# Optimization experiments

Measured on AMD Instinct MI355X. Metric: run time of the kernel, lower is better.

## Reference

```python
import jax, jax.numpy as jnp
import numpy as np

EMB, HEADS = 1024, 16
S = EMB // HEADS  # per-head dim = 64


def setup_inputs() -> dict:
    key = jax.random.key(0)
    ks = jax.random.split(key, 7)
    b, t = 2, 2048
    sc = 0.02
    return {
        "x": jax.random.normal(ks[0], (b, t, EMB), jnp.float32),
        "W_down": jax.random.normal(ks[1], (EMB, EMB), jnp.float32) * sc,
        "tokeys": jax.random.normal(ks[2], (HEADS, S, S), jnp.float32) * sc,
        "toqueries": jax.random.normal(ks[3], (HEADS, S, S), jnp.float32) * sc,
        "tovalues": jax.random.normal(ks[4], (HEADS, S, S), jnp.float32) * sc,
        "W_unify": jax.random.normal(ks[5], (EMB, EMB), jnp.float32) * sc,
        "b_unify": jax.random.normal(ks[6], (EMB,), jnp.float32) * sc,
    }


def reference(x, W_down, tokeys, toqueries, tovalues, W_unify, b_unify):
    b, t, e = x.shape
    h, s = HEADS, S
    scale = s ** (-0.25)
    # downproj (bias-free linear), split into heads: [b,t,h,s]
    xd = (x @ W_down).reshape(b, t, h, s)
    # per-head s x s projections
    keys = jnp.einsum("bthk,hik->bthi", xd, tokeys) * scale
    queries = jnp.einsum("bthk,hik->bthi", xd, toqueries) * scale
    values = jnp.einsum("bthk,hik->bthi", xd, tovalues)
    # attention: scores [b,h,q,k]
    dot = jnp.einsum("bqhs,bkhs->bhqk", queries, keys)
    attn = jax.nn.softmax(dot, axis=-1)
    out = jnp.einsum("bhqk,bkhs->bqhs", attn, values).reshape(b, t, e)
    return out @ W_unify + b_unify
```

## Files before the change

### kernel.cpp

```cpp
#include <hip/hip_runtime.h>

#define EMB   1024
#define HEADS 16
#define SDIM  64
#define BATCH 2
#define TSEQ  2048
#define BT    (BATCH*TSEQ)
#define NBH   (BATCH*HEADS)

typedef __attribute__((ext_vector_type(8))) short short8;
typedef __attribute__((ext_vector_type(4))) float f32x4;

static __device__ __forceinline__ unsigned short f2bf(float f) {
  unsigned u = __builtin_bit_cast(unsigned, f);
  u = (u + 0x7FFFu + ((u >> 16) & 1u)) >> 16;
  return (unsigned short)u;
}

#define MFMA(a, b, c) __builtin_amdgcn_mfma_f32_16x16x32_bf16((a), (b), (c), 0, 0, 0)

#define GLOAD_LDS16(g, l)                                                     \
  __builtin_amdgcn_global_load_lds(                                           \
      (const __attribute__((address_space(1))) unsigned*)(g),                 \
      (__attribute__((address_space(3))) unsigned*)(l), 16, 0, 0)

__global__ __launch_bounds__(256) void convert_kernel(
    const float* __restrict__ x,
    const float* __restrict__ tk, const float* __restrict__ tq,
    const float* __restrict__ tv,
    unsigned short* __restrict__ xb,
    unsigned short* __restrict__ pk, unsigned short* __restrict__ pq,
    unsigned short* __restrict__ pv) {
  const int NX4 = BT * EMB / 4;
  const int NP4 = HEADS * SDIM * SDIM / 4;
  int i = blockIdx.x * blockDim.x + threadIdx.x;
  const float* src; unsigned short* dst; int off;
  if (i < NX4)               { src = x;  dst = xb; off = i * 4; }
  else if (i < NX4 + NP4)    { src = tk; dst = pk; off = (i - NX4) * 4; }
  else if (i < NX4 + 2*NP4)  { src = tq; dst = pq; off = (i - NX4 - NP4) * 4; }
  else if (i < NX4 + 3*NP4)  { src = tv; dst = pv; off = (i - NX4 - 2*NP4) * 4; }
  else return;
  float4 v = *(const float4*)(src + off);
  ushort4 o;
  o.x = f2bf(v.x); o.y = f2bf(v.y); o.z = f2bf(v.z); o.w = f2bf(v.w);
  *(ushort4*)(dst + off) = o;
}

__global__ __launch_bounds__(256) void transpose_w_kernel(
    const float* __restrict__ w0, const float* __restrict__ w1,
    unsigned short* __restrict__ o0, unsigned short* __restrict__ o1) {
  __shared__ float tile[32][33];
  const float* in        = blockIdx.z ? w1 : w0;
  unsigned short* out    = blockIdx.z ? o1 : o0;
  int r0 = blockIdx.y * 32, c0 = blockIdx.x * 32;
  int tid = threadIdx.x;
  int r = tid >> 3, c4 = (tid & 7) * 4;
  float4 v = *(const float4*)(in + (size_t)(r0 + r) * EMB + c0 + c4);
  tile[r][c4 + 0] = v.x; tile[r][c4 + 1] = v.y;
  tile[r][c4 + 2] = v.z; tile[r][c4 + 3] = v.w;
  __syncthreads();
  ushort4 o;
  o.x = f2bf(tile[c4 + 0][r]);
  o.y = f2bf(tile[c4 + 1][r]);
  o.z = f2bf(tile[c4 + 2][r]);
  o.w = f2bf(tile[c4 + 3][r]);
  *(ushort4*)(out + (size_t)(c0 + r) * EMB + r0 + c4) = o;
}

template <int MODE>
__global__ __launch_bounds__(256) void gemm_bt_kernel(
    const unsigned short* __restrict__ A,
    const unsigned short* __restrict__ Bt,
    unsigned short* __restrict__ Cbf, float* __restrict__ Cf,
    const float* __restrict__ bias) {
  __shared__ short As[64 * 32];
  __shared__ short Bs[128 * 32];
  const int tid = threadIdx.x;
  const int lane = tid & 63;
  const int w = __builtin_amdgcn_readfirstlane(tid >> 6);
  const int wr = w >> 1, wc = w & 1;
  const int l15 = lane & 15, l4 = lane >> 4;
  const int flat = blockIdx.y * gridDim.x + blockIdx.x;
  const int vid = (flat & 7) * 64 + (flat >> 3);
  const int m0 = (vid >> 3) * 64;
  const int n0 = (vid & 7) * 128;
  const int lrow = lane >> 2, lcol = (lane & 3) * 8;
  f32x4 acc[2][4] = {};
  for (int kt = 0; kt < 32; ++kt) {
    const int k0 = kt * 32;
    for (int i = 0; i < 3; ++i) {
      int c = w * 3 + i;
      if (c < 4) {
        GLOAD_LDS16(A + (size_t)(m0 + c * 16 + lrow) * EMB + k0 + lcol,
                    &As[c * 512]);
      } else {
        int cb = c - 4;
        GLOAD_LDS16(Bt + (size_t)(n0 + cb * 16 + lrow) * EMB + k0 + lcol,
                    &Bs[cb * 512]);
      }
    }
    __syncthreads();
    short8 af[2], bf[4];
    for (int mi = 0; mi < 2; ++mi)
      af[mi] = *(short8*)&As[(wr * 32 + mi * 16 + l15) * 32 + l4 * 8];
    for (int ni = 0; ni < 4; ++ni)
      bf[ni] = *(short8*)&Bs[(wc * 64 + ni * 16 + l15) * 32 + l4 * 8];
    __builtin_amdgcn_s_setprio(1);
    for (int mi = 0; mi < 2; ++mi)
      for (int ni = 0; ni < 4; ++ni)
        acc[mi][ni] = MFMA(af[mi], bf[ni], acc[mi][ni]);
    __builtin_amdgcn_s_setprio(0);
    __syncthreads();
  }
  for (int mi = 0; mi < 2; ++mi)
    for (int ni = 0; ni < 4; ++ni) {
      int col = n0 + wc * 64 + ni * 16 + l15;
      for (int r = 0; r < 4; ++r) {
        int row = m0 + wr * 32 + mi * 16 + l4 * 4 + r;
        if (MODE == 0)
          Cbf[(size_t)row * EMB + col] = f2bf(acc[mi][ni][r]);
        else
          Cf[(size_t)row * EMB + col] = acc[mi][ni][r] + bias[col];
      }
    }
}

__global__ __launch_bounds__(256) void proj_qkv_kernel(
    const unsigned short* __restrict__ XD,
    const unsigned short* __restrict__ PK, const unsigned short* __restrict__ PQ,
    const unsigned short* __restrict__ PV,
    unsigned short* __restrict__ Qg, unsigned short* __restrict__ Kg,
    unsigned short* __restrict__ Vt) {
  __shared__ short xs[64 * 72];
  __shared__ short ps[3][64 * 72];
  const int tid = threadIdx.x, lane = tid & 63;
  const int w = __builtin_amdgcn_readfirstlane(tid >> 6);
  const int tt = blockIdx.x, bh = blockIdx.y;
  const int b = bh >> 4, h = bh & 15;
  const int l15 = lane & 15, l4 = lane >> 4;
  const unsigned short* srcs[3] = {PK + h * 4096, PQ + h * 4096, PV + h * 4096};
  for (int u = tid; u < 512; u += 256) {
    int row = u >> 3, ch = (u & 7) * 8;
    *(short8*)&xs[row * 72 + ch] = *(const short8*)(
        XD + (size_t)(b * TSEQ + tt * 64 + row) * EMB + h * 64 + ch);
  }
  for (int m = 0; m < 3; ++m)
    for (int u = tid; u < 512; u += 256) {
      int row = u >> 3, ch = (u & 7) * 8;
      *(short8*)&ps[m][row * 72 + ch] = *(const short8*)(srcs[m] + row * 64 + ch);
    }
  __syncthreads();
  short8 af[2];
  af[0] = *(short8*)&xs[(w * 16 + l15) * 72 + l4 * 8];
  af[1] = *(short8*)&xs[(w * 16 + l15) * 72 + 32 + l4 * 8];
  f32x4 aK[4] = {}, aQ[4] = {}, aV[4] = {};
  for (int ni = 0; ni < 4; ++ni)
    for (int kc = 0; kc < 2; ++kc) {
      short8 bk = *(short8*)&ps[0][(ni * 16 + l15) * 72 + kc * 32 + l4 * 8];
      short8 bq = *(short8*)&ps[1][(ni * 16 + l15) * 72 + kc * 32 + l4 * 8];
      short8 bv = *(short8*)&ps[2][(ni * 16 + l15) * 72 + kc * 32 + l4 * 8];
      aK[ni] = MFMA(af[kc], bk, aK[ni]);
      aQ[ni] = MFMA(af[kc], bq, aQ[ni]);
      aV[ni] = MFMA(af[kc], bv, aV[ni]);
    }
  for (int ni = 0; ni < 4; ++ni)
    for (int r = 0; r < 4; ++r) {
      int t = tt * 64 + w * 16 + l4 * 4 + r;
      size_t o = (size_t)(bh * TSEQ + t) * SDIM + ni * 16 + l15;
      Qg[o] = f2bf(aQ[ni][r]);
      Kg[o] = f2bf(aK[ni][r]);
    }
  __syncthreads();
  for (int ni = 0; ni < 4; ++ni)
    for (int r = 0; r < 4; ++r)
      xs[(w * 16 + l4 * 4 + r) * 72 + ni * 16 + l15] = (short)f2bf(aV[ni][r]);
  __syncthreads();
  for (int u = tid; u < 512; u += 256) {
    int d = u >> 3, ch = (u & 7) * 8;
    short8 v;
    for (int e = 0; e < 8; ++e) v[e] = xs[(ch + e) * 72 + d];
    *(short8*)(Vt + (size_t)(bh * 64 + d) * TSEQ + tt * 64 + ch) = v;
  }
}

__global__ __launch_bounds__(256) void attn_kernel(
    const unsigned short* __restrict__ Qg, const unsigned short* __restrict__ Kg,
    const unsigned short* __restrict__ Vt, unsigned short* __restrict__ Og) {
  __shared__ short Ks[2][64 * 64];
  __shared__ short Vs[2][64 * 64];
  __shared__ short Ps[4][16 * 64];
  const int tid = threadIdx.x, lane = tid & 63;
  const int w = __builtin_amdgcn_readfirstlane(tid >> 6);
  const int flat = blockIdx.y * gridDim.x + blockIdx.x;
  const int vid = (flat & 7) * 128 + (flat >> 3);
  const int qt = vid & 31, bh = vid >> 5;
  const int b = bh >> 4, h = bh & 15;
  const int l15 = lane & 15, l4 = lane >> 4;
  short8 qf[2];
  {
    int row = qt * 64 + w * 16 + l15;
    const unsigned short* qp = Qg + (size_t)(bh * TSEQ + row) * SDIM;
    qf[0] = *(const short8*)(qp + l4 * 8);
    qf[1] = *(const short8*)(qp + 32 + l4 * 8);
  }
  const unsigned short* Kbase = Kg + (size_t)bh * TSEQ * SDIM;
  const unsigned short* Vbase = Vt + (size_t)bh * SDIM * TSEQ;
  const int ur = tid >> 3, uc = (tid & 7);
  float lsum[4] = {0.f, 0.f, 0.f, 0.f};
  f32x4 O[4] = {};
  short8 rk0, rk1, rv0, rv1;
  auto loadKV = [&](int kt) {
    rk0 = *(const short8*)(Kbase + (size_t)(kt * 64 + ur) * SDIM + uc * 8);
    rk1 = *(const short8*)(Kbase + (size_t)(kt * 64 + ur + 32) * SDIM + uc * 8);
    rv0 = *(const short8*)(Vbase + (size_t)ur * TSEQ + kt * 64 + uc * 8);
    rv1 = *(const short8*)(Vbase + (size_t)(ur + 32) * TSEQ + kt * 64 + uc * 8);
  };
  auto storeKV = [&](int c) {
    char* KB = (char*)Ks[c]; char* VB = (char*)Vs[c];
    const int chB = uc * 16;
    *(short8*)(KB + ((ur * 128 + chB) ^ ((ur & 7) << 4)))        = rk0;
    *(short8*)(KB + (((ur + 32) * 128 + chB) ^ ((ur & 7) << 4))) = rk1;
    *(short8*)(VB + ((ur * 128 + chB) ^ ((ur & 7) << 4)))        = rv0;
    *(short8*)(VB + (((ur + 32) * 128 + chB) ^ ((ur & 7) << 4))) = rv1;
  };
  loadKV(0);
  storeKV(0);
  int cur = 0;
  char* PB = (char*)Ps[w];
  for (int kt = 0; kt < 32; ++kt) {
    __syncthreads();
    if (kt < 31) loadKV(kt + 1);
    char* KB = (char*)Ks[cur]; char* VB = (char*)Vs[cur];
    f32x4 s[4] = {};
    __builtin_amdgcn_s_setprio(1);
    for (int ni = 0; ni < 4; ++ni) {
      int j = ni * 16 + l15, sw = (j & 7) << 4;
      short8 kf0 = *(short8*)(KB + ((j * 128 + l4 * 16) ^ sw));
      short8 kf1 = *(short8*)(KB + ((j * 128 + 64 + l4 * 16) ^ sw));
      s[ni] = MFMA(qf[0], kf0, s[ni]);
      s[ni] = MFMA(qf[1], kf1, s[ni]);
    }
    __builtin_amdgcn_s_setprio(0);
    for (int ni = 0; ni < 4; ++ni)
      for (int r = 0; r < 4; ++r) {
        float p = __expf(s[ni][r] * 0.125f);
        lsum[r] += p;
        int row = l4 * 4 + r;
        *(unsigned short*)(PB + ((row * 128 + (ni * 16 + l15) * 2) ^
                                 ((row & 7) << 4))) = f2bf(p);
      }
    short8 pf0, pf1;
    {
      int sw = (l15 & 7) << 4;
      pf0 = *(short8*)(PB + ((l15 * 128 + l4 * 16) ^ sw));
      pf1 = *(short8*)(PB + ((l15 * 128 + 64 + l4 * 16) ^ sw));
    }
    __builtin_amdgcn_s_setprio(1);
    for (int ni = 0; ni < 4; ++ni) {
      int dd = ni * 16 + l15, sw = (dd & 7) << 4;
      short8 vf0 = *(short8*)(VB + ((dd * 128 + l4 * 16) ^ sw));
      short8 vf1 = *(short8*)(VB + ((dd * 128 + 64 + l4 * 16) ^ sw));
      O[ni] = MFMA(pf0, vf0, O[ni]);
      O[ni] = MFMA(pf1, vf1, O[ni]);
    }
    __builtin_amdgcn_s_setprio(0);
    if (kt < 31) storeKV(cur ^ 1);
    cur ^= 1;
  }
  for (int r = 0; r < 4; ++r) {
    float t = lsum[r];
    t += __shfl_xor(t, 1); t += __shfl_xor(t, 2);
    t += __shfl_xor(t, 4); t += __shfl_xor(t, 8);
    float inv = 1.0f / t;
    int trow = qt * 64 + w * 16 + l4 * 4 + r;
    for (int ni = 0; ni < 4; ++ni)
      Og[(size_t)(b * TSEQ + trow) * EMB + h * 64 + ni * 16 + l15] =
          f2bf(O[ni][r] * inv);
  }
}

extern "C" void kernel_launch(void* const* d_in, const int* in_sizes, int n_in,
                              void* d_out, int out_size, void* d_ws, size_t ws_size,
                              hipStream_t stream) {
  const float* x  = (const float*)d_in[0];
  const float* Wd = (const float*)d_in[1];
  const float* tk = (const float*)d_in[2];
  const float* tq = (const float*)d_in[3];
  const float* tv = (const float*)d_in[4];
  const float* Wu = (const float*)d_in[5];
  const float* bu = (const float*)d_in[6];
  float* out = (float*)d_out;

  char* ws = (char*)d_ws;
  size_t off = 0;
  auto alloc = [&](size_t bytes) {
    void* p = ws + off;
    off += (bytes + 255) & ~(size_t)255;
    return p;
  };
  unsigned short* XB  = (unsigned short*)alloc((size_t)BT * EMB * 2);
  unsigned short* WDT = (unsigned short*)alloc((size_t)EMB * EMB * 2);
  unsigned short* WUT = (unsigned short*)alloc((size_t)EMB * EMB * 2);
  unsigned short* PKb = (unsigned short*)alloc((size_t)HEADS * SDIM * SDIM * 2);
  unsigned short* PQb = (unsigned short*)alloc((size_t)HEADS * SDIM * SDIM * 2);
  unsigned short* PVb = (unsigned short*)alloc((size_t)HEADS * SDIM * SDIM * 2);
  unsigned short* XD  = (unsigned short*)alloc((size_t)BT * EMB * 2);
  unsigned short* Qg  = (unsigned short*)alloc((size_t)NBH * TSEQ * SDIM * 2);
  unsigned short* Kg  = (unsigned short*)alloc((size_t)NBH * TSEQ * SDIM * 2);
  unsigned short* Vtr = (unsigned short*)alloc((size_t)NBH * SDIM * TSEQ * 2);
  unsigned short* Og  = (unsigned short*)alloc((size_t)BT * EMB * 2);

  const int NX4 = BT * EMB / 4, NP4 = HEADS * SDIM * SDIM / 4;
  int nconv = (NX4 + 3 * NP4 + 255) / 256;
  convert_kernel<<<nconv, 256, 0, stream>>>(x, tk, tq, tv, XB, PKb, PQb, PVb);
  transpose_w_kernel<<<dim3(32, 32, 2), 256, 0, stream>>>(Wd, Wu, WDT, WUT);
  gemm_bt_kernel<0><<<dim3(8, 64), 256, 0, stream>>>(XB, WDT, XD, nullptr, nullptr);
  proj_qkv_kernel<<<dim3(32, 32), 256, 0, stream>>>(XD, PKb, PQb, PVb, Qg, Kg, Vtr);
  attn_kernel<<<dim3(32, 32), 256, 0, stream>>>(Qg, Kg, Vtr, Og);
  gemm_bt_kernel<1><<<dim3(8, 64), 256, 0, stream>>>(Og, WUT, nullptr, out, bu);
}
```

Measured before the change: 205.0 us.

## Stream K/V fragments from global into registers and double query rows per warp

The attention kernel no longer stages K and V tiles through shared memory. Each wave now loads its MFMA K/V fragments straight from global memory into registers, prefetching the next tile, and computes 32 query rows instead of 16, so the grid is halved. Keys are permuted so that four probabilities can be packed into a single 8-byte LDS store, and exp is folded into exp2 with a combined constant. The V-transpose write in the projection kernel is also reworked to use vector LDS reads. The trade-off is that every wave fetches the same K/V data from global memory (relying on cache hits), register pressure rises under launch_bounds(256,2), and bf16 rounding becomes round-half-up.

Result: slower. 250.6 us (+22.3%).

```diff
diff --git a/kernel.cpp b/kernel.cpp
--- a/kernel.cpp
+++ b/kernel.cpp
@@ -10,11 +10,15 @@
 
 typedef __attribute__((ext_vector_type(8))) short short8;
 typedef __attribute__((ext_vector_type(4))) float f32x4;
+typedef __attribute__((ext_vector_type(2))) unsigned u32x2;
 
 static __device__ __forceinline__ unsigned short f2bf(float f) {
   unsigned u = __builtin_bit_cast(unsigned, f);
   u = (u + 0x7FFFu + ((u >> 16) & 1u)) >> 16;
   return (unsigned short)u;
+}
+static __device__ __forceinline__ unsigned bfrnd(float a) {
+  return __builtin_bit_cast(unsigned, a) + 0x8000u;
 }
 
 #define MFMA(a, b, c) __builtin_amdgcn_mfma_f32_16x16x32_bf16((a), (b), (c), 0, 0, 0)
@@ -173,110 +177,102 @@
   __syncthreads();
   for (int ni = 0; ni < 4; ++ni)
     for (int r = 0; r < 4; ++r)
-      xs[(w * 16 + l4 * 4 + r) * 72 + ni * 16 + l15] = (short)f2bf(aV[ni][r]);
+      xs[(ni * 16 + l15) * 72 + (w * 16 + l4 * 4 + r)] = (short)f2bf(aV[ni][r]);
   __syncthreads();
   for (int u = tid; u < 512; u += 256) {
     int d = u >> 3, ch = (u & 7) * 8;
-    short8 v;
-    for (int e = 0; e < 8; ++e) v[e] = xs[(ch + e) * 72 + d];
+    short8 v = *(short8*)&xs[d * 72 + ch];
     *(short8*)(Vt + (size_t)(bh * 64 + d) * TSEQ + tt * 64 + ch) = v;
   }
 }
 
-__global__ __launch_bounds__(256) void attn_kernel(
+__global__ __launch_bounds__(256, 2) void attn_kernel(
     const unsigned short* __restrict__ Qg, const unsigned short* __restrict__ Kg,
     const unsigned short* __restrict__ Vt, unsigned short* __restrict__ Og) {
-  __shared__ short Ks[2][64 * 64];
-  __shared__ short Vs[2][64 * 64];
-  __shared__ short Ps[4][16 * 64];
+  __shared__ short Ps[4][32 * 64];
   const int tid = threadIdx.x, lane = tid & 63;
   const int w = __builtin_amdgcn_readfirstlane(tid >> 6);
-  const int flat = blockIdx.y * gridDim.x + blockIdx.x;
-  const int vid = (flat & 7) * 128 + (flat >> 3);
-  const int qt = vid & 31, bh = vid >> 5;
+  const int flat = blockIdx.y * 16 + blockIdx.x;
+  const int vid = (flat & 7) * 64 + (flat >> 3);
+  const int qt = vid & 15, bh = vid >> 4;
   const int b = bh >> 4, h = bh & 15;
   const int l15 = lane & 15, l4 = lane >> 4;
-  short8 qf[2];
-  {
-    int row = qt * 64 + w * 16 + l15;
-    const unsigned short* qp = Qg + (size_t)(bh * TSEQ + row) * SDIM;
-    qf[0] = *(const short8*)(qp + l4 * 8);
-    qf[1] = *(const short8*)(qp + 32 + l4 * 8);
-  }
-  const unsigned short* Kbase = Kg + (size_t)bh * TSEQ * SDIM;
-  const unsigned short* Vbase = Vt + (size_t)bh * SDIM * TSEQ;
-  const int ur = tid >> 3, uc = (tid & 7);
-  float lsum[4] = {0.f, 0.f, 0.f, 0.f};
-  f32x4 O[4] = {};
-  short8 rk0, rk1, rv0, rv1;
-  auto loadKV = [&](int kt) {
-    rk0 = *(const short8*)(Kbase + (size_t)(kt * 64 + ur) * SDIM + uc * 8);
-    rk1 = *(const short8*)(Kbase + (size_t)(kt * 64 + ur + 32) * SDIM + uc * 8);
-    rv0 = *(const short8*)(Vbase + (size_t)ur * TSEQ + kt * 64 + uc * 8);
-    rv1 = *(const short8*)(Vbase + (size_t)(ur + 32) * TSEQ + kt * 64 + uc * 8);
-  };
-  auto storeKV = [&](int c) {
-    char* KB = (char*)Ks[c]; char* VB = (char*)Vs[c];
-    const int chB = uc * 16;
-    *(short8*)(KB + ((ur * 128 + chB) ^ ((ur & 7) << 4)))        = rk0;
-    *(short8*)(KB + (((ur + 32) * 128 + chB) ^ ((ur & 7) << 4))) = rk1;
-    *(short8*)(VB + ((ur * 128 + chB) ^ ((ur & 7) << 4)))        = rv0;
-    *(short8*)(VB + (((ur + 32) * 128 + chB) ^ ((ur & 7) << 4))) = rv1;
-  };
-  loadKV(0);
-  storeKV(0);
-  int cur = 0;
+  const int qbase = qt * 128 + w * 32;
+  short8 qf[2][2];
+  for (int h2 = 0; h2 < 2; ++h2) {
+    const unsigned short* qp =
+        Qg + (size_t)(bh * TSEQ + qbase + h2 * 16 + l15) * SDIM;
+    qf[h2][0] = *(const short8*)(qp + l4 * 8);
+    qf[h2][1] = *(const short8*)(qp + 32 + l4 * 8);
+  }
+  const unsigned short* Kp =
+      Kg + (size_t)bh * TSEQ * SDIM + (size_t)(4 * l15) * SDIM + l4 * 8;
+  const unsigned short* Vp =
+      Vt + (size_t)bh * SDIM * TSEQ + (size_t)l15 * TSEQ + l4 * 8;
+  short8 kf[4][2], vf[4][2];
+  for (int ni = 0; ni < 4; ++ni)
+    for (int kc = 0; kc < 2; ++kc) {
+      kf[ni][kc] = *(const short8*)(Kp + ni * SDIM + kc * 32);
+      vf[ni][kc] = *(const short8*)(Vp + (size_t)ni * 16 * TSEQ + kc * 32);
+    }
+  float lsum[2][4] = {};
+  f32x4 O[2][4] = {};
   char* PB = (char*)Ps[w];
+  const float CEXP = 0.18033688011112042f;
   for (int kt = 0; kt < 32; ++kt) {
-    __syncthreads();
-    if (kt < 31) loadKV(kt + 1);
-    char* KB = (char*)Ks[cur]; char* VB = (char*)Vs[cur];
-    f32x4 s[4] = {};
-    __builtin_amdgcn_s_setprio(1);
-    for (int ni = 0; ni < 4; ++ni) {
-      int j = ni * 16 + l15, sw = (j & 7) << 4;
-      short8 kf0 = *(short8*)(KB + ((j * 128 + l4 * 16) ^ sw));
-      short8 kf1 = *(short8*)(KB + ((j * 128 + 64 + l4 * 16) ^ sw));
-      s[ni] = MFMA(qf[0], kf0, s[ni]);
-      s[ni] = MFMA(qf[1], kf1, s[ni]);
-    }
-    __builtin_amdgcn_s_setprio(0);
-    for (int ni = 0; ni < 4; ++ni)
+    __builtin_amdgcn_s_barrier();
+    for (int h2 = 0; h2 < 2; ++h2) {
+      f32x4 s[4] = {};
+      for (int ni = 0; ni < 4; ++ni) {
+        s[ni] = MFMA(qf[h2][0], kf[ni][0], s[ni]);
+        s[ni] = MFMA(qf[h2][1], kf[ni][1], s[ni]);
+      }
       for (int r = 0; r < 4; ++r) {
-        float p = __expf(s[ni][r] * 0.125f);
-        lsum[r] += p;
-        int row = l4 * 4 + r;
-        *(unsigned short*)(PB + ((row * 128 + (ni * 16 + l15) * 2) ^
-                                 ((row & 7) << 4))) = f2bf(p);
-      }
-    short8 pf0, pf1;
-    {
-      int sw = (l15 & 7) << 4;
-      pf0 = *(short8*)(PB + ((l15 * 128 + l4 * 16) ^ sw));
-      pf1 = *(short8*)(PB + ((l15 * 128 + 64 + l4 * 16) ^ sw));
-    }
-    __builtin_amdgcn_s_setprio(1);
-    for (int ni = 0; ni < 4; ++ni) {
-      int dd = ni * 16 + l15, sw = (dd & 7) << 4;
-      short8 vf0 = *(short8*)(VB + ((dd * 128 + l4 * 16) ^ sw));
-      short8 vf1 = *(short8*)(VB + ((dd * 128 + 64 + l4 * 16) ^ sw));
-      O[ni] = MFMA(pf0, vf0, O[ni]);
-      O[ni] = MFMA(pf1, vf1, O[ni]);
-    }
-    __builtin_amdgcn_s_setprio(0);
-    if (kt < 31) storeKV(cur ^ 1);
-    cur ^= 1;
-  }
-  for (int r = 0; r < 4; ++r) {
-    float t = lsum[r];
-    t += __shfl_xor(t, 1); t += __shfl_xor(t, 2);
-    t += __shfl_xor(t, 4); t += __shfl_xor(t, 8);
-    float inv = 1.0f / t;
-    int trow = qt * 64 + w * 16 + l4 * 4 + r;
-    for (int ni = 0; ni < 4; ++ni)
-      Og[(size_t)(b * TSEQ + trow) * EMB + h * 64 + ni * 16 + l15] =
-          f2bf(O[ni][r] * inv);
-  }
+        float p0 = exp2f(s[0][r] * CEXP);
+        float p1 = exp2f(s[1][r] * CEXP);
+        float p2 = exp2f(s[2][r] * CEXP);
+        float p3 = exp2f(s[3][r] * CEXP);
+        lsum[h2][r] += (p0 + p1) + (p2 + p3);
+        u32x2 pk;
+        pk[0] = __builtin_amdgcn_perm(bfrnd(p1), bfrnd(p0), 0x07060302u);
+        pk[1] = __builtin_amdgcn_perm(bfrnd(p3), bfrnd(p2), 0x07060302u);
+        int row = h2 * 16 + l4 * 4 + r;
+        *(u32x2*)(PB + ((row * 128 + l15 * 8) ^ ((row & 7) << 4))) = pk;
+      }
+    }
+    if (kt < 31)
+      for (int ni = 0; ni < 4; ++ni)
+        for (int kc = 0; kc < 2; ++kc)
+          kf[ni][kc] = *(const short8*)(Kp + (size_t)(kt + 1) * 64 * SDIM +
+                                        ni * SDIM + kc * 32);
+    short8 pf[2][2];
+    for (int h2 = 0; h2 < 2; ++h2) {
+      int row = h2 * 16 + l15, sw = (l15 & 7) << 4;
+      pf[h2][0] = *(short8*)(PB + ((row * 128 + l4 * 16) ^ sw));
+      pf[h2][1] = *(short8*)(PB + ((row * 128 + 64 + l4 * 16) ^ sw));
+    }
+    for (int h2 = 0; h2 < 2; ++h2)
+      for (int ni = 0; ni < 4; ++ni) {
+        O[h2][ni] = MFMA(pf[h2][0], vf[ni][0], O[h2][ni]);
+        O[h2][ni] = MFMA(pf[h2][1], vf[ni][1], O[h2][ni]);
+      }
+    if (kt < 31)
+      for (int ni = 0; ni < 4; ++ni)
+        for (int kc = 0; kc < 2; ++kc)
+          vf[ni][kc] = *(const short8*)(Vp + (size_t)ni * 16 * TSEQ +
+                                        (kt + 1) * 64 + kc * 32);
+  }
+  for (int h2 = 0; h2 < 2; ++h2)
+    for (int r = 0; r < 4; ++r) {
+      float t = lsum[h2][r];
+      t += __shfl_xor(t, 1); t += __shfl_xor(t, 2);
+      t += __shfl_xor(t, 4); t += __shfl_xor(t, 8);
+      float inv = 1.0f / t;
+      int trow = qbase + h2 * 16 + l4 * 4 + r;
+      for (int ni = 0; ni < 4; ++ni)
+        Og[(size_t)(b * TSEQ + trow) * EMB + h * 64 + ni * 16 + l15] =
+            f2bf(O[h2][ni][r] * inv);
+    }
 }
 
 extern "C" void kernel_launch(void* const* d_in, const int* in_sizes, int n_in,
@@ -316,6 +312,6 @@
   transpose_w_kernel<<<dim3(32, 32, 2), 256, 0, stream>>>(Wd, Wu, WDT, WUT);
   gemm_bt_kernel<0><<<dim3(8, 64), 256, 0, stream>>>(XB, WDT, XD, nullptr, nullptr);
   proj_qkv_kernel<<<dim3(32, 32), 256, 0, stream>>>(XD, PKb, PQb, PVb, Qg, Kg, Vtr);
-  attn_kernel<<<dim3(32, 32), 256, 0, stream>>>(Qg, Kg, Vtr, Og);
+  attn_kernel<<<dim3(16, 32), 256, 0, stream>>>(Qg, Kg, Vtr, Og);
   gemm_bt_kernel<1><<<dim3(8, 64), 256, 0, stream>>>(Og, WUT, nullptr, out, bu);
 }
```
